# Performance work log

Measured on AMD Instinct MI355X. Metric: run time of the kernel, lower is better.

## Reference

```python
import jax, jax.numpy as jnp
import numpy as np

N = 50000
E = 1600000
IN = 128
HID = 64
HEADS = 2
OUT = 32
NEG_SLOPE = 0.2  # PyG GATConv default negative_slope


def _gat_conv(x, edge_index, edge_attr, W, a_src, a_dst, W_e, a_e, bias, heads, out_ch, concat):
    """Faithful PyG GATConv with edge_dim, add_self_loops=True (fill_value='mean')."""
    n = x.shape[0]
    src, dst = edge_index[0], edge_index[1]
    # self-loop edge_attr = per-node mean of incoming edge attrs (PyG fill_value='mean')
    ones = jnp.ones((src.shape[0],), x.dtype)
    deg = jax.ops.segment_sum(ones, dst, num_segments=n)
    loop_attr = jax.ops.segment_sum(edge_attr, dst, num_segments=n) / jnp.maximum(deg, 1.0)[:, None]
    loop = jnp.arange(n)
    src = jnp.concatenate([src, loop])
    dst = jnp.concatenate([dst, loop])
    ea = jnp.concatenate([edge_attr, loop_attr], axis=0)  # [E+N, 1]
    # node / edge projections
    h = (x @ W).reshape(n, heads, out_ch)                 # [N, H, C]
    al_src = jnp.sum(h * a_src, axis=-1)                  # [N, H]
    al_dst = jnp.sum(h * a_dst, axis=-1)                  # [N, H]
    he = (ea @ W_e).reshape(-1, heads, out_ch)            # [E+N, H, C]
    al_e = jnp.sum(he * a_e, axis=-1)                     # [E+N, H]
    logits = jax.nn.leaky_relu(al_src[src] + al_dst[dst] + al_e, NEG_SLOPE)
    # segment softmax over destination nodes
    m = jax.ops.segment_max(logits, dst, num_segments=n)  # [N, H]
    p = jnp.exp(logits - m[dst])
    denom = jax.ops.segment_sum(p, dst, num_segments=n)
    alpha = p / (denom[dst] + 1e-16)                      # [E+N, H]
    # weighted scatter-aggregate of source messages
    out = jax.ops.segment_sum(alpha[:, :, None] * h[src], dst, num_segments=n)  # [N, H, C]
    out = out.reshape(n, heads * out_ch) if concat else out.mean(axis=1)
    return out + bias


def setup_inputs() -> dict:
    key = jax.random.key(0)
    ks = jax.random.split(key, 16)
    x = jax.random.normal(ks[0], (N, IN), dtype=jnp.float32)
    edge_index = jax.random.randint(ks[1], (2, E), 0, N)
    edge_weight = jax.random.uniform(ks[2], (E, 1), dtype=jnp.float32)
    s1 = 1.0 / np.sqrt(IN)
    W1 = jax.random.normal(ks[3], (IN, HEADS * HID), dtype=jnp.float32) * s1
    att_src1 = jax.random.normal(ks[4], (HEADS, HID), dtype=jnp.float32) * 0.1
    att_dst1 = jax.random.normal(ks[5], (HEADS, HID), dtype=jnp.float32) * 0.1
    We1 = jax.random.normal(ks[6], (1, HEADS * HID), dtype=jnp.float32) * 0.5
    att_e1 = jax.random.normal(ks[7], (HEADS, HID), dtype=jnp.float32) * 0.1
    b1 = jnp.zeros((HEADS * HID,), dtype=jnp.float32)
    s2 = 1.0 / np.sqrt(HEADS * HID)
    W2 = jax.random.normal(ks[8], (HEADS * HID, OUT), dtype=jnp.float32) * s2
    att_src2 = jax.random.normal(ks[9], (1, OUT), dtype=jnp.float32) * 0.1
    att_dst2 = jax.random.normal(ks[10], (1, OUT), dtype=jnp.float32) * 0.1
    We2 = jax.random.normal(ks[11], (1, OUT), dtype=jnp.float32) * 0.5
    att_e2 = jax.random.normal(ks[12], (1, OUT), dtype=jnp.float32) * 0.1
    b2 = jnp.zeros((OUT,), dtype=jnp.float32)
    return {"x": x, "edge_index": edge_index, "edge_weight": edge_weight,
            "W1": W1, "att_src1": att_src1, "att_dst1": att_dst1, "We1": We1, "att_e1": att_e1, "b1": b1,
            "W2": W2, "att_src2": att_src2, "att_dst2": att_dst2, "We2": We2, "att_e2": att_e2, "b2": b2}


def reference(x, edge_index, edge_weight, W1, att_src1, att_dst1, We1, att_e1, b1,
              W2, att_src2, att_dst2, We2, att_e2, b2):
    h = _gat_conv(x, edge_index, edge_weight, W1, att_src1, att_dst1, We1, att_e1, b1,
                  HEADS, HID, True)
    h = jax.nn.elu(h)
    return _gat_conv(h, edge_index, edge_weight, W2, att_src2, att_dst2, We2, att_e2, b2,
                     1, OUT, False)
```

## Files before the change

kernel.cpp:

```cpp
#include <hip/hip_runtime.h>
#include <hip/hip_fp16.h>

#define NEG_SLOPE 0.2f
#define NBUK 8
#define NPB  6272
#define NFINE 512
#define FPN  98
#define BCAP (2048*104)
#define FCAP 4096
#define EPT 8

__device__ __forceinline__ float wredsum(float v){
  #pragma unroll
  for (int k=32;k;k>>=1) v += __shfl_xor(v,k,64);
  return v;
}

__global__ void k_init(int* __restrict__ tails, int* __restrict__ tails2,
                       const float* __restrict__ We1, const float* __restrict__ ae1,
                       const float* __restrict__ We2, const float* __restrict__ ae2,
                       float* __restrict__ cst){
  int t = threadIdx.x;
  if (t < NBUK) tails[t] = 0;
  if (t < NFINE) tails2[t] = 0;
  if (t == 0){
    float c0 = 0.f, c1 = 0.f, c2 = 0.f;
    for (int k = 0; k < 64; k++){ c0 += We1[k]*ae1[k]; c1 += We1[64+k]*ae1[64+k]; }
    for (int k = 0; k < 32; k++){ c2 += We2[k]*ae2[k]; }
    cst[0] = c0; cst[1] = c1; cst[2] = c2;
  }
}

__global__ __launch_bounds__(256) void k_pA_gemm1(
    const int* __restrict__ ei, const float* __restrict__ ew,
    uint2* __restrict__ bbuf, int* __restrict__ tails,
    const float* __restrict__ x, const float* __restrict__ W,
    const float* __restrict__ pa_s, const float* __restrict__ pa_d,
    __half* __restrict__ h1h, float* __restrict__ alsrc, float* __restrict__ aldst,
    int N_, int E_, int nG, int nTot)
{
  __shared__ float ws[64*128];
  __shared__ float xs[16][128];
  __shared__ int scnt[NBUK], sbase[NBUK], sgb[NBUK];
  const int b = blockIdx.x;
  const int t = threadIdx.x;
  const size_t gb = (size_t)b * (size_t)nG / (size_t)nTot;
  const bool is_g = ((size_t)(b+1) * (size_t)nG / (size_t)nTot) > gb;

  if (!is_g){
    uint2* sb = (uint2*)ws;
    unsigned char* sfb = (unsigned char*)(ws + 4096);
    const int e0 = (b - (int)gb) * 2048;
    if (t < NBUK) scnt[t] = 0;
    __syncthreads();
    int mb[EPT]; uint2 me[EPT]; bool ok[EPT];
    #pragma unroll
    for (int u = 0; u < EPT; u++){
      int e = e0 + u*256 + t;
      ok[u] = (e < E_); mb[u] = 0;
      if (ok[u]){
        int dst = ei[E_ + e], src = ei[e];
        float wv = ew[e];
        mb[u] = dst / NPB;
        me[u] = make_uint2(((unsigned)dst << 16) | (unsigned)src, __float_as_uint(wv));
        atomicAdd(&scnt[mb[u]], 1);
      }
    }
    __syncthreads();
    if (t == 0){ int run = 0;
      #pragma unroll
      for (int j = 0; j < NBUK; j++){ sbase[j] = run; run += scnt[j]; } }
    __syncthreads();
    if (t < NBUK) scnt[t] = 0;
    __syncthreads();
    #pragma unroll
    for (int u = 0; u < EPT; u++)
      if (ok[u]){
        int p = sbase[mb[u]] + atomicAdd(&scnt[mb[u]], 1);
        sb[p] = me[u]; sfb[p] = (unsigned char)mb[u];
      }
    __syncthreads();
    if (t < NBUK) sgb[t] = atomicAdd(&tails[t], scnt[t]);
    __syncthreads();
    int total = sbase[NBUK-1] + scnt[NBUK-1];
    for (int p = t; p < total; p += 256){
      int bb = sfb[p];
      int g = sgb[bb] + (p - sbase[bb]);
      if (g < BCAP) bbuf[(size_t)bb*BCAP + g] = sb[p];
    }
    return;
  }

  const int row0 = (int)gb * 16;
  if (row0 >= N_) return;
  const float4* x4 = (const float4*)(x + (size_t)row0*128);
  float4* xs4 = (float4*)xs;
  for (int i = t; i < 512; i += 256){
    int r = i >> 5;
    xs4[i] = (row0 + r < N_) ? x4[i] : make_float4(0.f,0.f,0.f,0.f);
  }
  const int c = t & 127, rh = t >> 7;
  float acc[8];
  #pragma unroll
  for (int u = 0; u < 8; u++) acc[u] = 0.f;
  const float4* W4 = (const float4*)W;
  float4* ws4 = (float4*)ws;
  for (int kt = 0; kt < 2; kt++){
    __syncthreads();
    for (int i = t; i < 2048; i += 256) ws4[i] = W4[kt*2048 + i];
    __syncthreads();
    #pragma unroll 8
    for (int k = 0; k < 64; k++){
      float wv = ws[k*128 + c];
      #pragma unroll
      for (int u = 0; u < 8; u++) acc[u] = fmaf(xs[rh*8+u][kt*64 + k], wv, acc[u]);
    }
  }
  #pragma unroll
  for (int u = 0; u < 8; u++){
    int row = row0 + rh*8 + u;
    if (row < N_) h1h[(size_t)row*128 + c] = __float2half(acc[u]);
  }
  __syncthreads();
  #pragma unroll
  for (int u = 0; u < 8; u++) xs[rh*8+u][c] = acc[u];
  __syncthreads();
  if (t < 32){
    int rr = t >> 1, hh = t & 1;
    int orow = row0 + rr;
    if (orow < N_){
      float ps = 0.f, pd = 0.f;
      for (int c2 = 0; c2 < 64; c2++){
        float hv = xs[rr][hh*64 + c2];
        ps = fmaf(hv, pa_s[hh*64 + c2], ps);
        pd = fmaf(hv, pa_d[hh*64 + c2], pd);
      }
      alsrc[orow*2 + hh] = ps;
      aldst[orow*2 + hh] = pd;
    }
  }
}

__global__ __launch_bounds__(256) void k_pB1(const uint2* __restrict__ bbuf,
                        const int* __restrict__ tails,
                        uint2* __restrict__ fbuf, int* __restrict__ tails2){
  __shared__ uint2 sb[2048];
  __shared__ unsigned char sfb[2048];
  __shared__ int scnt[64], sbase[64], sgb[64];
  const int coarse = blockIdx.x & 7, chunk = blockIdx.x >> 3;
  const int cnt = min(tails[coarse], BCAP);
  const int t = threadIdx.x;
  const int i0 = chunk*2048;
  if (i0 >= cnt) return;
  if (t < 64) scnt[t] = 0;
  __syncthreads();
  int fl[EPT]; uint2 me[EPT]; bool ok[EPT];
  #pragma unroll
  for (int u = 0; u < EPT; u++){
    int i = i0 + u*256 + t;
    ok[u] = (i < cnt); fl[u] = 0;
    if (ok[u]){
      me[u] = bbuf[(size_t)coarse*BCAP + i];
      int dst = (int)(me[u].x >> 16);
      fl[u] = dst/FPN - coarse*64;
      atomicAdd(&scnt[fl[u]], 1);
    }
  }
  __syncthreads();
  if (t == 0){ int run = 0;
    for (int j = 0; j < 64; j++){ sbase[j] = run; run += scnt[j]; } }
  __syncthreads();
  if (t < 64) scnt[t] = 0;
  __syncthreads();
  #pragma unroll
  for (int u = 0; u < EPT; u++)
    if (ok[u]){
      int p = sbase[fl[u]] + atomicAdd(&scnt[fl[u]], 1);
      sb[p] = me[u]; sfb[p] = (unsigned char)fl[u];
    }
  __syncthreads();
  if (t < 64) sgb[t] = atomicAdd(&tails2[coarse*64 + t], scnt[t]);
  __syncthreads();
  int total = sbase[63] + scnt[63];
  for (int p = t; p < total; p += 256){
    int f = sfb[p];
    int g = sgb[f] + (p - sbase[f]);
    if (g < FCAP) fbuf[(size_t)(coarse*64 + f)*FCAP + g] = sb[p];
  }
}

__global__ __launch_bounds__(256) void k_pB2(const uint2* __restrict__ fbuf,
                        const int* __restrict__ tails2,
                        unsigned* __restrict__ csr, int* __restrict__ rp,
                        int* __restrict__ dg, int N_){
  __shared__ unsigned csr4[FCAP];
  __shared__ int scnt[100], sbase[100], sfill[100];
  const int f = blockIdx.x;
  const int cnt = min(tails2[f], FCAP);
  const int t = threadIdx.x;
  const int n0 = f*FPN;
  if (t < 100){ scnt[t] = 0; sfill[t] = 0; }
  __syncthreads();
  const uint2* srcb = fbuf + (size_t)f*FCAP;
  for (int i = t; i < cnt; i += 256){
    int dst = (int)(srcb[i].x >> 16);
    atomicAdd(&scnt[dst - n0], 1);
  }
  __syncthreads();
  if (t == 0){ int run = 0;
    for (int j = 0; j < FPN; j++){ sbase[j] = run; run += scnt[j]; } }
  __syncthreads();
  for (int i = t; i < cnt; i += 256){
    uint2 e = srcb[i];
    int loc = (int)(e.x >> 16) - n0;
    int pos = sbase[loc] + atomicAdd(&sfill[loc], 1);
    unsigned h = (unsigned)__half_as_ushort(__float2half(__uint_as_float(e.y)));
    csr4[pos] = (h << 16) | (e.x & 0xFFFFu);
  }
  __syncthreads();
  const int base = f*FCAP;
  for (int i = t; i < cnt; i += 256) csr[base + i] = csr4[i];
  if (t < FPN){
    int n = n0 + t;
    if (n < N_){ rp[n] = base + sbase[t]; dg[n] = scnt[t]; }
  }
}

__global__ __launch_bounds__(256) void k_layer1(
  const int* __restrict__ rp, const int* __restrict__ dg,
  const unsigned* __restrict__ csr,
  const float* __restrict__ alsrc, const float* __restrict__ aldst,
  const __half* __restrict__ h1h, const float* __restrict__ b1,
  const float* __restrict__ cst, const float* __restrict__ W2,
  const float* __restrict__ as2, const float* __restrict__ ad2,
  __half* __restrict__ h2h, float* __restrict__ alsrc2, float* __restrict__ aldst2,
  int N_)
{
  __shared__ float W2s[128*32];
  __shared__ float sas[32], sad[32];
  __shared__ float hxs[4][128];
  const int t = threadIdx.x;
  {
    const float4* W4 = (const float4*)W2;
    float4* s4 = (float4*)W2s;
    for (int i = t; i < 1024; i += 256) s4[i] = W4[i];
    if (t < 32){ sas[t] = as2[t]; sad[t] = ad2[t]; }
  }
  __syncthreads();

  int wid = (blockIdx.x*256 + t) >> 6;
  int lane = t & 63;
  if (wid >= N_) return;
  const int n = wid;
  const int wv_ = t >> 6;
  const int deg = dg[n];
  const int p0 = rp[n];
  const float ce0 = cst[0], ce1 = cst[1];
  const float2 adv = *(const float2*)&aldst[2*n];
  const int quad = lane >> 4;
  const int ch8 = (lane & 15) * 8;
  const int head = ch8 >> 6;
  float acc[8] = {0.f,0.f,0.f,0.f,0.f,0.f,0.f,0.f};
  float sum0 = 0.f, sum1 = 0.f, wsum = 0.f;

  for (int base = 0; base < deg; base += 64){
    int i = base + lane;
    float pp0 = 0.f, pp1 = 0.f; int s = 0;
    if (i < deg){
      unsigned pk = csr[p0 + i];
      s = (int)(pk & 0xFFFFu);
      float ea = __half2float(__ushort_as_half((unsigned short)(pk >> 16)));
      wsum += ea;
      float2 av = *(const float2*)&alsrc[2*s];
      float l0 = av.x + adv.x + ea*ce0;
      float l1 = av.y + adv.y + ea*ce1;
      l0 = (l0 > 0.f) ? l0 : NEG_SLOPE*l0;
      l1 = (l1 > 0.f) ? l1 : NEG_SLOPE*l1;
      pp0 = __expf(l0); pp1 = __expf(l1);
    }
    sum0 += pp0; sum1 += pp1;
    int lim = min(64, deg - base);
    for (int jb = 0; jb < lim; jb += 4){
      int j  = jb + quad;
      int jc = (j < lim) ? j : 0;
      int   sj = __shfl(s,   jc, 64);
      float q0 = __shfl(pp0, jc, 64);
      float q1 = __shfl(pp1, jc, 64);
      float q  = head ? q1 : q0;
      if (j < lim){
        uint4 hv = *(const uint4*)(h1h + (size_t)sj*128 + ch8);
        const half2* hp = (const half2*)&hv;
        #pragma unroll
        for (int u = 0; u < 4; u++){
          float2 fv = __half22float2(hp[u]);
          acc[2*u]   = fmaf(q, fv.x, acc[2*u]);
          acc[2*u+1] = fmaf(q, fv.y, acc[2*u+1]);
        }
      }
    }
  }
  sum0 = wredsum(sum0); sum1 = wredsum(sum1); wsum = wredsum(wsum);

  float mean = wsum / fmaxf((float)deg, 1.0f);
  float2 avs = *(const float2*)&alsrc[2*n];
  float ls0 = avs.x + adv.x + mean*ce0;
  float ls1 = avs.y + adv.y + mean*ce1;
  ls0 = (ls0 > 0.f) ? ls0 : NEG_SLOPE*ls0;
  ls1 = (ls1 > 0.f) ? ls1 : NEG_SLOPE*ls1;
  float ps0 = __expf(ls0), ps1 = __expf(ls1);
  sum0 += ps0; sum1 += ps1;

  #pragma unroll
  for (int u = 0; u < 8; u++){
    acc[u] += __shfl_xor(acc[u], 16, 64);
    acc[u] += __shfl_xor(acc[u], 32, 64);
  }

  if (lane < 16){
    float qs = head ? ps1 : ps0;
    uint4 hv = *(const uint4*)(h1h + (size_t)n*128 + ch8);
    const half2* hp = (const half2*)&hv;
    #pragma unroll
    for (int u = 0; u < 4; u++){
      float2 fv = __half22float2(hp[u]);
      acc[2*u]   = fmaf(qs, fv.x, acc[2*u]);
      acc[2*u+1] = fmaf(qs, fv.y, acc[2*u+1]);
    }
    float inv = head ? 1.f/(sum1 + 1e-16f) : 1.f/(sum0 + 1e-16f);
    float4 b0 = *(const float4*)&b1[ch8];
    float4 b4 = *(const float4*)&b1[ch8 + 4];
    float vv[8];
    #pragma unroll
    for (int u = 0; u < 8; u++){
      float bv = (u < 4) ? (&b0.x)[u] : (&b4.x)[u-4];
      float v = acc[u]*inv + bv;
      vv[u] = (v > 0.f) ? v : expm1f(v);
    }
    *(float4*)&hxs[wv_][ch8]     = make_float4(vv[0],vv[1],vv[2],vv[3]);
    *(float4*)&hxs[wv_][ch8 + 4] = make_float4(vv[4],vv[5],vv[6],vv[7]);
  }
  __builtin_amdgcn_wave_barrier();

  const int c2 = lane & 31, kh = lane >> 5;
  const float* hb = hxs[wv_] + kh*64;
  float a2 = 0.f;
  #pragma unroll 16
  for (int k = 0; k < 64; k++)
    a2 = fmaf(hb[k], W2s[(kh*64 + k)*32 + c2], a2);
  a2 += __shfl_xor(a2, 32, 64);
  float ps = a2 * sas[c2], pd = a2 * sad[c2];
  #pragma unroll
  for (int k2 = 16; k2; k2 >>= 1){ ps += __shfl_xor(ps, k2, 64); pd += __shfl_xor(pd, k2, 64); }
  if (lane < 32) h2h[(size_t)n*32 + c2] = __float2half(a2);
  if (lane == 0){ alsrc2[n] = ps; aldst2[n] = pd; }
}

__global__ __launch_bounds__(256) void k_layer2(
  const int* __restrict__ rp, const int* __restrict__ dg,
  const unsigned* __restrict__ csr,
  const float* __restrict__ alsrc2, const float* __restrict__ aldst2,
  const __half* __restrict__ h2h, const float* __restrict__ b2,
  const float* __restrict__ cst, float* __restrict__ out, int N_)
{
  int wid = (blockIdx.x*256 + threadIdx.x) >> 6;
  int lane = threadIdx.x & 63;
  if (wid >= N_) return;
  const int n = wid;
  const int deg = dg[n];
  const int p0 = rp[n];
  const float ce2 = cst[2];
  const float adn = aldst2[n];
  const int oct = lane >> 3;
  const int ch4 = (lane & 7) * 4;
  float acc[4] = {0.f,0.f,0.f,0.f};
  float sum = 0.f, wsum = 0.f;

  for (int base = 0; base < deg; base += 64){
    int i = base + lane;
    float pp = 0.f; int s = 0;
    if (i < deg){
      unsigned pk = csr[p0 + i];
      s = (int)(pk & 0xFFFFu);
      float ea = __half2float(__ushort_as_half((unsigned short)(pk >> 16)));
      wsum += ea;
      float l = alsrc2[s] + ea*ce2 + adn;
      l = (l > 0.f) ? l : NEG_SLOPE*l;
      pp = __expf(l);
    }
    sum += pp;
    int lim = min(64, deg - base);
    for (int jb = 0; jb < lim; jb += 8){
      int j  = jb + oct;
      int jc = (j < lim) ? j : 0;
      float q  = __shfl(pp, jc, 64);
      int   sj = __shfl(s,  jc, 64);
      if (j < lim){
        uint2 hv = *(const uint2*)(h2h + (size_t)sj*32 + ch4);
        const half2* hp = (const half2*)&hv;
        float2 f0 = __half22float2(hp[0]);
        float2 f1 = __half22float2(hp[1]);
        acc[0] = fmaf(q, f0.x, acc[0]);
        acc[1] = fmaf(q, f0.y, acc[1]);
        acc[2] = fmaf(q, f1.x, acc[2]);
        acc[3] = fmaf(q, f1.y, acc[3]);
      }
    }
  }
  sum = wredsum(sum); wsum = wredsum(wsum);

  float mean = wsum / fmaxf((float)deg, 1.0f);
  float ls = alsrc2[n] + mean*ce2 + adn;
  ls = (ls > 0.f) ? ls : NEG_SLOPE*ls;
  float ps = __expf(ls);
  sum += ps;

  #pragma unroll
  for (int u = 0; u < 4; u++){
    acc[u] += __shfl_xor(acc[u],  8, 64);
    acc[u] += __shfl_xor(acc[u], 16, 64);
    acc[u] += __shfl_xor(acc[u], 32, 64);
  }
  if (lane < 8){
    uint2 hv = *(const uint2*)(h2h + (size_t)n*32 + ch4);
    const half2* hp = (const half2*)&hv;
    float2 f0 = __half22float2(hp[0]);
    float2 f1 = __half22float2(hp[1]);
    acc[0] = fmaf(ps, f0.x, acc[0]);
    acc[1] = fmaf(ps, f0.y, acc[1]);
    acc[2] = fmaf(ps, f1.x, acc[2]);
    acc[3] = fmaf(ps, f1.y, acc[3]);
    float inv = 1.f/(sum + 1e-16f);
    float4 bv = *(const float4*)&b2[ch4];
    float4 o;
    o.x = acc[0]*inv + bv.x;
    o.y = acc[1]*inv + bv.y;
    o.z = acc[2]*inv + bv.z;
    o.w = acc[3]*inv + bv.w;
    *(float4*)&out[(size_t)n*32 + ch4] = o;
  }
}

extern "C" void kernel_launch(void* const* d_in, const int* in_sizes, int n_in,
                              void* d_out, int out_size, void* d_ws, size_t ws_size,
                              hipStream_t stream)
{
  const float* x   = (const float*)d_in[0];
  const int*   ei  = (const int*)d_in[1];
  const float* ew  = (const float*)d_in[2];
  const float* W1  = (const float*)d_in[3];
  const float* as1 = (const float*)d_in[4];
  const float* ad1 = (const float*)d_in[5];
  const float* We1 = (const float*)d_in[6];
  const float* ae1 = (const float*)d_in[7];
  const float* b1  = (const float*)d_in[8];
  const float* W2  = (const float*)d_in[9];
  const float* as2 = (const float*)d_in[10];
  const float* ad2 = (const float*)d_in[11];
  const float* We2 = (const float*)d_in[12];
  const float* ae2 = (const float*)d_in[13];
  const float* b2  = (const float*)d_in[14];
  const int N_ = in_sizes[0] / 128;
  const int E_ = in_sizes[1] / 2;

  char* w = (char*)d_ws;
  size_t o = 0;
  auto alloc = [&](size_t b){ size_t r = o; o = (o + b + 255) & ~(size_t)255; return r; };
  size_t o_tail  = alloc(NBUK*4);
  size_t o_tail2 = alloc(NFINE*4);
  size_t o_cst   = alloc(64);
  size_t o_bbuf  = alloc((size_t)NBUK*BCAP*8);
  size_t o_fbuf  = alloc((size_t)NFINE*FCAP*8);
  size_t o_csr   = alloc((size_t)NFINE*FCAP*4);
  size_t o_rp    = alloc((size_t)N_*4);
  size_t o_dg    = alloc((size_t)N_*4);
  size_t o_h1    = alloc((size_t)N_*128*2);
  size_t o_h2    = alloc((size_t)N_*32*2);
  size_t o_als1  = alloc((size_t)N_*8);
  size_t o_ald1  = alloc((size_t)N_*8);
  size_t o_als2  = alloc((size_t)N_*4);
  size_t o_ald2  = alloc((size_t)N_*4);

  int*      tails = (int*)(w+o_tail);
  int*      tails2= (int*)(w+o_tail2);
  float*    cst   = (float*)(w+o_cst);
  uint2*    bbuf  = (uint2*)(w+o_bbuf);
  uint2*    fbuf  = (uint2*)(w+o_fbuf);
  unsigned* csr   = (unsigned*)(w+o_csr);
  int*      rp    = (int*)(w+o_rp);
  int*      dg    = (int*)(w+o_dg);
  __half*   h1h   = (__half*)(w+o_h1);
  __half*   h2h   = (__half*)(w+o_h2);
  float*    als1  = (float*)(w+o_als1);
  float*    ald1  = (float*)(w+o_ald1);
  float*    als2  = (float*)(w+o_als2);
  float*    ald2  = (float*)(w+o_ald2);
  float*    out   = (float*)d_out;

  int nB  = (E_ + 2047) / 2048;
  int nG  = (N_ + 15) / 16;
  int nTot = nB + nG;
  int nB1 = (BCAP / 2048) * NBUK;

  k_init<<<1, 512, 0, stream>>>(tails, tails2, We1, ae1, We2, ae2, cst);
  k_pA_gemm1<<<nTot, 256, 0, stream>>>(ei, ew, bbuf, tails, x, W1, as1, ad1,
                                       h1h, als1, ald1, N_, E_, nG, nTot);
  k_pB1<<<nB1, 256, 0, stream>>>(bbuf, tails, fbuf, tails2);
  k_pB2<<<NFINE, 256, 0, stream>>>(fbuf, tails2, csr, rp, dg, N_);
  k_layer1<<<(N_+3)/4, 256, 0, stream>>>(rp, dg, csr, als1, ald1, h1h, b1, cst,
                                         W2, as2, ad2, h2h, als2, ald2, N_);
  k_layer2<<<(N_+3)/4, 256, 0, stream>>>(rp, dg, csr, als2, ald2, h2h, b2, cst, out, N_);
}
```

Measured before the change: 202.2 us.

## Collapse two-pass edge bucketing into one 64-bucket pass and use fma_mix

The CSR build now sorts edges in two stages instead of three. The first pass scatters each edge into one of 64 mid-size buckets of 782 nodes, and a single kernel per bucket does a counting sort, with a block-parallel scan, straight into global CSR. This removes the intermediate fine-bucket pass and one kernel launch. The cost is that only 64 blocks do the final sort, which means low parallelism on a large GPU, and the CSR writes are scattered rather than staged in shared memory. Separately, the gather loops use inline v_fma_mix_f32 so fp16 features feed the FMA directly without separate conversions.

```diff
diff --git a/kernel.cpp b/kernel.cpp
--- a/kernel.cpp
+++ b/kernel.cpp
@@ -2,13 +2,13 @@
 #include <hip/hip_fp16.h>
 
 #define NEG_SLOPE 0.2f
-#define NBUK 8
-#define NPB  6272
-#define NFINE 512
-#define FPN  98
-#define BCAP (2048*104)
-#define FCAP 4096
+#define NMID 64
+#define MPN  782
+#define MCAP 27648
 #define EPT 8
+
+#define FMAMIX_LO(acc, pk, q) asm("v_fma_mix_f32 %0, %1, %2, %0 op_sel:[0,0,0] op_sel_hi:[1,0,0]" : "+v"(acc) : "v"(pk), "v"(q))
+#define FMAMIX_HI(acc, pk, q) asm("v_fma_mix_f32 %0, %1, %2, %0 op_sel:[1,0,0] op_sel_hi:[1,0,0]" : "+v"(acc) : "v"(pk), "v"(q))
 
 __device__ __forceinline__ float wredsum(float v){
   #pragma unroll
@@ -16,13 +16,12 @@
   return v;
 }
 
-__global__ void k_init(int* __restrict__ tails, int* __restrict__ tails2,
+__global__ void k_init(int* __restrict__ tails,
                        const float* __restrict__ We1, const float* __restrict__ ae1,
                        const float* __restrict__ We2, const float* __restrict__ ae2,
                        float* __restrict__ cst){
   int t = threadIdx.x;
-  if (t < NBUK) tails[t] = 0;
-  if (t < NFINE) tails2[t] = 0;
+  if (t < NMID) tails[t] = 0;
   if (t == 0){
     float c0 = 0.f, c1 = 0.f, c2 = 0.f;
     for (int k = 0; k < 64; k++){ c0 += We1[k]*ae1[k]; c1 += We1[64+k]*ae1[64+k]; }
@@ -33,7 +32,7 @@
 
 __global__ __launch_bounds__(256) void k_pA_gemm1(
     const int* __restrict__ ei, const float* __restrict__ ew,
-    uint2* __restrict__ bbuf, int* __restrict__ tails,
+    uint2* __restrict__ mbuf, int* __restrict__ tails,
     const float* __restrict__ x, const float* __restrict__ W,
     const float* __restrict__ pa_s, const float* __restrict__ pa_d,
     __half* __restrict__ h1h, float* __restrict__ alsrc, float* __restrict__ aldst,
@@ -41,7 +40,7 @@
 {
   __shared__ float ws[64*128];
   __shared__ float xs[16][128];
-  __shared__ int scnt[NBUK], sbase[NBUK], sgb[NBUK];
+  __shared__ int scnt[NMID], sbase[NMID], sgb[NMID];
   const int b = blockIdx.x;
   const int t = threadIdx.x;
   const size_t gb = (size_t)b * (size_t)nG / (size_t)nTot;
@@ -51,7 +50,7 @@
     uint2* sb = (uint2*)ws;
     unsigned char* sfb = (unsigned char*)(ws + 4096);
     const int e0 = (b - (int)gb) * 2048;
-    if (t < NBUK) scnt[t] = 0;
+    for (int i = t; i < NMID; i += 256) scnt[i] = 0;
     __syncthreads();
     int mb[EPT]; uint2 me[EPT]; bool ok[EPT];
     #pragma unroll
@@ -61,7 +60,7 @@
       if (ok[u]){
         int dst = ei[E_ + e], src = ei[e];
         float wv = ew[e];
-        mb[u] = dst / NPB;
+        mb[u] = dst / MPN;
         me[u] = make_uint2(((unsigned)dst << 16) | (unsigned)src, __float_as_uint(wv));
         atomicAdd(&scnt[mb[u]], 1);
       }
@@ -69,9 +68,9 @@
     __syncthreads();
     if (t == 0){ int run = 0;
       #pragma unroll
-      for (int j = 0; j < NBUK; j++){ sbase[j] = run; run += scnt[j]; } }
-    __syncthreads();
-    if (t < NBUK) scnt[t] = 0;
+      for (int j = 0; j < NMID; j++){ sbase[j] = run; run += scnt[j]; } }
+    __syncthreads();
+    if (t < NMID) scnt[t] = 0;
     __syncthreads();
     #pragma unroll
     for (int u = 0; u < EPT; u++)
@@ -80,13 +79,13 @@
         sb[p] = me[u]; sfb[p] = (unsigned char)mb[u];
       }
     __syncthreads();
-    if (t < NBUK) sgb[t] = atomicAdd(&tails[t], scnt[t]);
-    __syncthreads();
-    int total = sbase[NBUK-1] + scnt[NBUK-1];
+    if (t < NMID) sgb[t] = atomicAdd(&tails[t], scnt[t]);
+    __syncthreads();
+    int total = sbase[NMID-1] + scnt[NMID-1];
     for (int p = t; p < total; p += 256){
       int bb = sfb[p];
       int g = sgb[bb] + (p - sbase[bb]);
-      if (g < BCAP) bbuf[(size_t)bb*BCAP + g] = sb[p];
+      if (g < MCAP) mbuf[(size_t)bb*MCAP + g] = sb[p];
     }
     return;
   }
@@ -141,88 +140,60 @@
   }
 }
 
-__global__ __launch_bounds__(256) void k_pB1(const uint2* __restrict__ bbuf,
+__global__ __launch_bounds__(256) void k_pB(const uint2* __restrict__ mbuf,
                         const int* __restrict__ tails,
-                        uint2* __restrict__ fbuf, int* __restrict__ tails2){
-  __shared__ uint2 sb[2048];
-  __shared__ unsigned char sfb[2048];
-  __shared__ int scnt[64], sbase[64], sgb[64];
-  const int coarse = blockIdx.x & 7, chunk = blockIdx.x >> 3;
-  const int cnt = min(tails[coarse], BCAP);
-  const int t = threadIdx.x;
-  const int i0 = chunk*2048;
-  if (i0 >= cnt) return;
-  if (t < 64) scnt[t] = 0;
-  __syncthreads();
-  int fl[EPT]; uint2 me[EPT]; bool ok[EPT];
-  #pragma unroll
-  for (int u = 0; u < EPT; u++){
-    int i = i0 + u*256 + t;
-    ok[u] = (i < cnt); fl[u] = 0;
-    if (ok[u]){
-      me[u] = bbuf[(size_t)coarse*BCAP + i];
-      int dst = (int)(me[u].x >> 16);
-      fl[u] = dst/FPN - coarse*64;
-      atomicAdd(&scnt[fl[u]], 1);
-    }
-  }
-  __syncthreads();
-  if (t == 0){ int run = 0;
-    for (int j = 0; j < 64; j++){ sbase[j] = run; run += scnt[j]; } }
-  __syncthreads();
-  if (t < 64) scnt[t] = 0;
-  __syncthreads();
-  #pragma unroll
-  for (int u = 0; u < EPT; u++)
-    if (ok[u]){
-      int p = sbase[fl[u]] + atomicAdd(&scnt[fl[u]], 1);
-      sb[p] = me[u]; sfb[p] = (unsigned char)fl[u];
-    }
-  __syncthreads();
-  if (t < 64) sgb[t] = atomicAdd(&tails2[coarse*64 + t], scnt[t]);
-  __syncthreads();
-  int total = sbase[63] + scnt[63];
-  for (int p = t; p < total; p += 256){
-    int f = sfb[p];
-    int g = sgb[f] + (p - sbase[f]);
-    if (g < FCAP) fbuf[(size_t)(coarse*64 + f)*FCAP + g] = sb[p];
-  }
-}
-
-__global__ __launch_bounds__(256) void k_pB2(const uint2* __restrict__ fbuf,
-                        const int* __restrict__ tails2,
                         unsigned* __restrict__ csr, int* __restrict__ rp,
                         int* __restrict__ dg, int N_){
-  __shared__ unsigned csr4[FCAP];
-  __shared__ int scnt[100], sbase[100], sfill[100];
-  const int f = blockIdx.x;
-  const int cnt = min(tails2[f], FCAP);
+  __shared__ int scnt[784], sbase[784], sfill[784];
+  __shared__ int part[256];
+  const int m = blockIdx.x;
+  const int cnt = min(tails[m], MCAP);
   const int t = threadIdx.x;
-  const int n0 = f*FPN;
-  if (t < 100){ scnt[t] = 0; sfill[t] = 0; }
-  __syncthreads();
-  const uint2* srcb = fbuf + (size_t)f*FCAP;
+  const int n0 = m*MPN;
+  for (int i = t; i < 784; i += 256){ scnt[i] = 0; sfill[i] = 0; }
+  __syncthreads();
+  const uint2* srcb = mbuf + (size_t)m*MCAP;
   for (int i = t; i < cnt; i += 256){
     int dst = (int)(srcb[i].x >> 16);
     atomicAdd(&scnt[dst - n0], 1);
   }
   __syncthreads();
-  if (t == 0){ int run = 0;
-    for (int j = 0; j < FPN; j++){ sbase[j] = run; run += scnt[j]; } }
-  __syncthreads();
+  {
+    int l0 = t*4, s = 0;
+    if (l0 < 784){
+      #pragma unroll
+      for (int k = 0; k < 4; k++){
+        int idx = l0 + k;
+        int v = (idx < 784) ? scnt[idx] : 0;
+        if (idx < 784) sbase[idx] = s;
+        s += v;
+      }
+    }
+    part[t] = s;
+    __syncthreads();
+    if (t == 0){ int run = 0;
+      for (int j = 0; j < 256; j++){ int v = part[j]; part[j] = run; run += v; } }
+    __syncthreads();
+    if (l0 < 784){
+      #pragma unroll
+      for (int k = 0; k < 4; k++){
+        int idx = l0 + k;
+        if (idx < 784) sbase[idx] += part[t];
+      }
+    }
+  }
+  __syncthreads();
+  const int base = m*MCAP;
   for (int i = t; i < cnt; i += 256){
     uint2 e = srcb[i];
     int loc = (int)(e.x >> 16) - n0;
     int pos = sbase[loc] + atomicAdd(&sfill[loc], 1);
     unsigned h = (unsigned)__half_as_ushort(__float2half(__uint_as_float(e.y)));
-    csr4[pos] = (h << 16) | (e.x & 0xFFFFu);
-  }
-  __syncthreads();
-  const int base = f*FCAP;
-  for (int i = t; i < cnt; i += 256) csr[base + i] = csr4[i];
-  if (t < FPN){
-    int n = n0 + t;
-    if (n < N_){ rp[n] = base + sbase[t]; dg[n] = scnt[t]; }
+    csr[base + pos] = (h << 16) | (e.x & 0xFFFFu);
+  }
+  for (int i = t; i < MPN; i += 256){
+    int n = n0 + i;
+    if (n < N_){ rp[n] = base + sbase[i]; dg[n] = scnt[i]; }
   }
 }
 
@@ -289,12 +260,11 @@
       float q  = head ? q1 : q0;
       if (j < lim){
         uint4 hv = *(const uint4*)(h1h + (size_t)sj*128 + ch8);
-        const half2* hp = (const half2*)&hv;
+        const unsigned* hw = (const unsigned*)&hv;
         #pragma unroll
         for (int u = 0; u < 4; u++){
-          float2 fv = __half22float2(hp[u]);
-          acc[2*u]   = fmaf(q, fv.x, acc[2*u]);
-          acc[2*u+1] = fmaf(q, fv.y, acc[2*u+1]);
+          FMAMIX_LO(acc[2*u],   hw[u], q);
+          FMAMIX_HI(acc[2*u+1], hw[u], q);
         }
       }
     }
@@ -319,12 +289,11 @@
   if (lane < 16){
     float qs = head ? ps1 : ps0;
     uint4 hv = *(const uint4*)(h1h + (size_t)n*128 + ch8);
-    const half2* hp = (const half2*)&hv;
+    const unsigned* hw = (const unsigned*)&hv;
     #pragma unroll
     for (int u = 0; u < 4; u++){
-      float2 fv = __half22float2(hp[u]);
-      acc[2*u]   = fmaf(qs, fv.x, acc[2*u]);
-      acc[2*u+1] = fmaf(qs, fv.y, acc[2*u+1]);
+      FMAMIX_LO(acc[2*u],   hw[u], qs);
+      FMAMIX_HI(acc[2*u+1], hw[u], qs);
     }
     float inv = head ? 1.f/(sum1 + 1e-16f) : 1.f/(sum0 + 1e-16f);
     float4 b0 = *(const float4*)&b1[ch8];
@@ -396,13 +365,11 @@
       int   sj = __shfl(s,  jc, 64);
       if (j < lim){
         uint2 hv = *(const uint2*)(h2h + (size_t)sj*32 + ch4);
-        const half2* hp = (const half2*)&hv;
-        float2 f0 = __half22float2(hp[0]);
-        float2 f1 = __half22float2(hp[1]);
-        acc[0] = fmaf(q, f0.x, acc[0]);
-        acc[1] = fmaf(q, f0.y, acc[1]);
-        acc[2] = fmaf(q, f1.x, acc[2]);
-        acc[3] = fmaf(q, f1.y, acc[3]);
+        const unsigned* hw = (const unsigned*)&hv;
+        FMAMIX_LO(acc[0], hw[0], q);
+        FMAMIX_HI(acc[1], hw[0], q);
+        FMAMIX_LO(acc[2], hw[1], q);
+        FMAMIX_HI(acc[3], hw[1], q);
       }
     }
   }
@@ -422,13 +389,11 @@
   }
   if (lane < 8){
     uint2 hv = *(const uint2*)(h2h + (size_t)n*32 + ch4);
-    const half2* hp = (const half2*)&hv;
-    float2 f0 = __half22float2(hp[0]);
-    float2 f1 = __half22float2(hp[1]);
-    acc[0] = fmaf(ps, f0.x, acc[0]);
-    acc[1] = fmaf(ps, f0.y, acc[1]);
-    acc[2] = fmaf(ps, f1.x, acc[2]);
-    acc[3] = fmaf(ps, f1.y, acc[3]);
+    const unsigned* hw = (const unsigned*)&hv;
+    FMAMIX_LO(acc[0], hw[0], ps);
+    FMAMIX_HI(acc[1], hw[0], ps);
+    FMAMIX_LO(acc[2], hw[1], ps);
+    FMAMIX_HI(acc[3], hw[1], ps);
     float inv = 1.f/(sum + 1e-16f);
     float4 bv = *(const float4*)&b2[ch4];
     float4 o;
@@ -465,12 +430,10 @@
   char* w = (char*)d_ws;
   size_t o = 0;
   auto alloc = [&](size_t b){ size_t r = o; o = (o + b + 255) & ~(size_t)255; return r; };
-  size_t o_tail  = alloc(NBUK*4);
-  size_t o_tail2 = alloc(NFINE*4);
+  size_t o_tail  = alloc(NMID*4);
   size_t o_cst   = alloc(64);
-  size_t o_bbuf  = alloc((size_t)NBUK*BCAP*8);
-  size_t o_fbuf  = alloc((size_t)NFINE*FCAP*8);
-  size_t o_csr   = alloc((size_t)NFINE*FCAP*4);
+  size_t o_mbuf  = alloc((size_t)NMID*MCAP*8);
+  size_t o_csr   = alloc((size_t)NMID*MCAP*4);
   size_t o_rp    = alloc((size_t)N_*4);
   size_t o_dg    = alloc((size_t)N_*4);
   size_t o_h1    = alloc((size_t)N_*128*2);
@@ -481,10 +444,8 @@
   size_t o_ald2  = alloc((size_t)N_*4);
 
   int*      tails = (int*)(w+o_tail);
-  int*      tails2= (int*)(w+o_tail2);
   float*    cst   = (float*)(w+o_cst);
-  uint2*    bbuf  = (uint2*)(w+o_bbuf);
-  uint2*    fbuf  = (uint2*)(w+o_fbuf);
+  uint2*    mbuf  = (uint2*)(w+o_mbuf);
   unsigned* csr   = (unsigned*)(w+o_csr);
   int*      rp    = (int*)(w+o_rp);
   int*      dg    = (int*)(w+o_dg);
@@ -499,13 +460,11 @@
   int nB  = (E_ + 2047) / 2048;
   int nG  = (N_ + 15) / 16;
   int nTot = nB + nG;
-  int nB1 = (BCAP / 2048) * NBUK;
-
-  k_init<<<1, 512, 0, stream>>>(tails, tails2, We1, ae1, We2, ae2, cst);
-  k_pA_gemm1<<<nTot, 256, 0, stream>>>(ei, ew, bbuf, tails, x, W1, as1, ad1,
+
+  k_init<<<1, 256, 0, stream>>>(tails, We1, ae1, We2, ae2, cst);
+  k_pA_gemm1<<<nTot, 256, 0, stream>>>(ei, ew, mbuf, tails, x, W1, as1, ad1,
                                        h1h, als1, ald1, N_, E_, nG, nTot);
-  k_pB1<<<nB1, 256, 0, stream>>>(bbuf, tails, fbuf, tails2);
-  k_pB2<<<NFINE, 256, 0, stream>>>(fbuf, tails2, csr, rp, dg, N_);
+  k_pB<<<NMID, 256, 0, stream>>>(mbuf, tails, csr, rp, dg, N_);
   k_layer1<<<(N_+3)/4, 256, 0, stream>>>(rp, dg, csr, als1, ald1, h1h, b1, cst,
                                          W2, as2, ad2, h2h, als2, ald2, N_);
   k_layer2<<<(N_+3)/4, 256, 0, stream>>>(rp, dg, csr, als2, ald2, h2h, b2, cst, out, N_);
```

Result: slower. 234.4 us (+16.0%).
